# Kernel optimization log

Hardware: AMD Instinct MI355X
Metric: run time of the kernel (lower is better)

The kernel has to match this reference:

```python
import jax, jax.numpy as jnp
import numpy as np

N = 100000   # nodes
E = 400000   # edges
R = 237      # relations
D = 200      # feature dim (dims=[200,200,200])
B = 4096     # triple batch
L = 2        # num GAT layers
ALPHA = 0.01 # leaky-relu slope


def setup_inputs() -> dict:
    key = jax.random.key(0)
    ks = jax.random.split(key, 11)
    return dict(
        ent_embed=jax.random.normal(ks[0], (N, D), jnp.float32),
        rel_embed=jax.random.normal(ks[1], (R, D), jnp.float32),
        W_gat=jax.random.normal(ks[2], (L, D, D), jnp.float32) * 0.1,
        att_a=jax.random.normal(ks[3], (L, 2 * D), jnp.float32) * 0.1,
        W_hw=jax.random.normal(ks[4], (D, D), jnp.float32) * 0.1,
        b_hw=jax.random.normal(ks[5], (1, D), jnp.float32) * 0.1,
        edge_src=jax.random.randint(ks[6], (E,), 0, N),
        edge_dst=jax.random.randint(ks[7], (E,), 0, N),
        batch_h=jax.random.randint(ks[8], (B,), 0, N),
        batch_r=jax.random.randint(ks[9], (B,), 0, R),
        batch_t=jax.random.randint(ks[10], (B,), 0, N),
    )


def _gat_layer(x, W, a, src, dst):
    # x: [N,D], W: [D,D], a: [2D]
    Wh = x @ W                                  # [N,D]
    s_src = Wh @ a[:D]                          # [N] source score
    s_dst = Wh @ a[D:]                          # [N] dest score
    e = jax.nn.leaky_relu(s_src[src] + s_dst[dst], ALPHA)  # [E]
    # segment softmax over incoming edges of each destination node
    m = jax.ops.segment_max(e, dst, num_segments=N)
    m = jax.lax.stop_gradient(jnp.where(jnp.isfinite(m), m, 0.0))
    ex = jnp.exp(e - m[dst])
    denom = jax.ops.segment_sum(ex, dst, num_segments=N)
    att = ex / jnp.maximum(denom[dst], 1e-9)    # [E]
    out = jax.ops.segment_sum(att[:, None] * Wh[src], dst, num_segments=N)  # [N,D]
    return jax.nn.sigmoid(out)                  # act = torch.sigmoid, 1 head, concat=False


def reference(ent_embed, rel_embed, W_gat, att_a, W_hw, b_hw,
              edge_src, edge_dst, batch_h, batch_r, batch_t):
    x = ent_embed
    for i in range(L):
        gat_out = _gat_layer(x, W_gat[i], att_a[i], edge_src, edge_dst)
        # highway gate: sigma = sigmoid(x W + b); shared W,b across layers
        sigma = jax.nn.sigmoid(x @ W_hw + b_hw)
        x = sigma * gat_out + (1.0 - sigma) * x
    h = x[batch_h]
    r = rel_embed[batch_r]
    t = x[batch_t]
    return (h, r, t)
```

## Files before the change

### kernel.cpp

```cpp
#include <hip/hip_runtime.h>
#include <math.h>

#define NNODES 100000
#define NEDGES 400000
#define DIM    200
#define NB     4096
#define NL     2
#define ALPHA  0.01f
#define D4     (DIM/4)
#define NPAD   100096
#define KPAD   224
#define NKS    7
#define NCF    26
#define NBB    (2*NB)
#define NBLK   ((NNODES + 255) / 256)
#define SCAN_BPB 1024
#define NSB    ((NNODES + SCAN_BPB - 1) / SCAN_BPB)

typedef __attribute__((ext_vector_type(8))) short short8;
typedef __attribute__((ext_vector_type(4))) float f32x4;

__device__ __forceinline__ float sigm(float v) { return 1.0f / (1.0f + expf(-v)); }
__device__ __forceinline__ unsigned short f2bf(float f) {
    unsigned u = __float_as_uint(f);
    unsigned r = u + 0x7fff + ((u >> 16) & 1);
    return (unsigned short)(r >> 16);
}
__device__ __forceinline__ float bflo(unsigned u) { return __uint_as_float(u << 16); }
__device__ __forceinline__ float bfhi(unsigned u) { return __uint_as_float(u & 0xffff0000u); }

__global__ __launch_bounds__(256) void zero_k(int* __restrict__ deg, int* __restrict__ mask,
                                              int* __restrict__ lbbuf)
{
    int i = blockIdx.x * 256 + threadIdx.x;
    if (i < NNODES) { deg[i] = 0; mask[i] = 0; }
    if (i < 320) lbbuf[i] = 0;
}

__global__ void hist_k(const int* __restrict__ dst, int* __restrict__ deg)
{
    int e = blockIdx.x * blockDim.x + threadIdx.x;
    if (e < NEDGES) atomicAdd(&deg[dst[e]], 1);
}

template<int MODE>
__global__ __launch_bounds__(256) void scanlb_k(const int* __restrict__ in,
                                                int* __restrict__ state,
                                                int* __restrict__ ticket,
                                                int* __restrict__ o0,
                                                int* __restrict__ o1,
                                                int* __restrict__ o2)
{
    __shared__ int sbid;
    __shared__ int tmp[256];
    __shared__ int sexcl;
    int tid = threadIdx.x;
    if (tid == 0) sbid = atomicAdd(ticket, 1);
    __syncthreads();
    int bid = sbid;
    int base = bid * SCAN_BPB + tid * 4;

    int4 v4 = make_int4(0, 0, 0, 0);
    if (base + 3 < NNODES) v4 = *(const int4*)(in + base);
    else {
        if (base + 0 < NNODES) v4.x = in[base + 0];
        if (base + 1 < NNODES) v4.y = in[base + 1];
        if (base + 2 < NNODES) v4.z = in[base + 2];
    }
    int s1 = v4.x + v4.y, s2 = s1 + v4.z, s3 = s2 + v4.w;

    tmp[tid] = s3; __syncthreads();
#pragma unroll
    for (int off = 1; off < 256; off <<= 1) {
        int t = (tid >= off) ? tmp[tid - off] : 0;
        __syncthreads();
        tmp[tid] += t;
        __syncthreads();
    }
    int bexcl_t = tmp[tid] - s3;
    int btotal  = tmp[255];

    if (tid == 0) {
        int st = (bid == 0) ? ((2 << 30) | btotal) : ((1 << 30) | btotal);
        __hip_atomic_store(&state[bid], st, __ATOMIC_RELEASE, __HIP_MEMORY_SCOPE_AGENT);
        if (bid == 0) sexcl = 0;
    }
    if (bid > 0 && tid < 64) {
        int excl = 0;
        int pred = bid - 1;
        while (pred >= -64) {
            int idx = pred - tid;
            int s = (idx >= 0)
                ? __hip_atomic_load(&state[idx], __ATOMIC_ACQUIRE, __HIP_MEMORY_SCOPE_AGENT)
                : (2 << 30);
            int f = ((unsigned)s) >> 30;
            unsigned long long nv = __ballot(f == 0);
            unsigned long long iv = __ballot(f == 2);
            int firstnv = nv ? (__ffsll(nv) - 1) : 64;
            int firstiv = iv ? (__ffsll(iv) - 1) : 64;
            if (firstiv < firstnv) {
                int contrib = (tid <= firstiv) ? (s & 0x3FFFFFFF) : 0;
#pragma unroll
                for (int m = 32; m; m >>= 1) contrib += __shfl_xor(contrib, m, 64);
                excl += contrib;
                break;
            } else if (firstnv > 0) {
                int contrib = (tid < firstnv) ? (s & 0x3FFFFFFF) : 0;
#pragma unroll
                for (int m = 32; m; m >>= 1) contrib += __shfl_xor(contrib, m, 64);
                excl += contrib;
                pred -= firstnv;
            }
        }
        if (tid == 0) {
            __hip_atomic_store(&state[bid], (2 << 30) | (excl + btotal),
                               __ATOMIC_RELEASE, __HIP_MEMORY_SCOPE_AGENT);
            sexcl = excl;
        }
    }
    __syncthreads();
    int ex = sexcl + bexcl_t;

    if (MODE == 0) {
        int4 r = make_int4(ex, ex + v4.x, ex + s1, ex + s2);
        if (base + 3 < NNODES) {
            *(int4*)(o0 + base) = r;
            *(int4*)(o1 + base) = r;
        } else {
            if (base + 0 < NNODES) { o0[base + 0] = r.x; o1[base + 0] = r.x; }
            if (base + 1 < NNODES) { o0[base + 1] = r.y; o1[base + 1] = r.y; }
            if (base + 2 < NNODES) { o0[base + 2] = r.z; o1[base + 2] = r.z; }
        }
        if (bid == NSB - 1 && tid == 0) o0[NNODES] = NEDGES;
    } else {
        int vv[4] = { v4.x, v4.y, v4.z, v4.w };
        int ee[4] = { ex, ex + v4.x, ex + s1, ex + s2 };
#pragma unroll
        for (int j = 0; j < 4; ++j) {
            int idx = base + j;
            if (idx < NNODES) {
                if (vv[j]) { o0[ee[j]] = idx; o1[idx] = ee[j]; }
                if (idx == NNODES - 1) *o2 = ee[j] + vv[j];
            }
        }
    }
}

__global__ void scatter_k(const int* __restrict__ src, const int* __restrict__ dst,
                          int* __restrict__ cursor, int* __restrict__ csr_src)
{
    int e = blockIdx.x * blockDim.x + threadIdx.x;
    if (e >= NEDGES) return;
    int d = dst[e];
    int p = atomicAdd(&cursor[d], 1);
    csr_src[p] = src[e];
}

__global__ void mark_k(const int* __restrict__ bh, const int* __restrict__ bt,
                       const int* __restrict__ rs, const int* __restrict__ csr_src,
                       int* __restrict__ mask)
{
    int e = blockIdx.x * 256 + threadIdx.x;
    if (e >= NBB) return;
    int node = (e < NB) ? bh[e] : bt[e - NB];
    mask[node] = 1;
    int b = rs[node], en = rs[node + 1];
    for (int j = b; j < en; ++j) mask[csr_src[j]] = 1;
}

__global__ __launch_bounds__(256) void convscore_k(const float* __restrict__ xin,
                                                   const float* __restrict__ wvl,
                                                   unsigned short* __restrict__ ap,
                                                   float* __restrict__ s_src,
                                                   float* __restrict__ s_dst)
{
    int gt = blockIdx.x * 256 + threadIdx.x;
    int row = gt >> 5, hl = gt & 31;
    if (row >= NPAD) return;

    float ps = 0.f, pd = 0.f;
    if (hl < 28) {
        uint4 o = make_uint4(0u, 0u, 0u, 0u);
        if (row < NNODES && hl < 25) {
            size_t base = (size_t)row * D4 + hl * 2;
            float4 x0 = ((const float4*)xin)[base];
            float4 x1 = ((const float4*)xin)[base + 1];
            o.x = (unsigned)f2bf(x0.x) | ((unsigned)f2bf(x0.y) << 16);
            o.y = (unsigned)f2bf(x0.z) | ((unsigned)f2bf(x0.w) << 16);
            o.z = (unsigned)f2bf(x1.x) | ((unsigned)f2bf(x1.y) << 16);
            o.w = (unsigned)f2bf(x1.z) | ((unsigned)f2bf(x1.w) << 16);
            float4 s0 = ((const float4*)wvl)[hl * 2];
            float4 s1 = ((const float4*)wvl)[hl * 2 + 1];
            float4 d0 = ((const float4*)(wvl + DIM))[hl * 2];
            float4 d1 = ((const float4*)(wvl + DIM))[hl * 2 + 1];
            ps = x0.x*s0.x + x0.y*s0.y + x0.z*s0.z + x0.w*s0.w
               + x1.x*s1.x + x1.y*s1.y + x1.z*s1.z + x1.w*s1.w;
            pd = x0.x*d0.x + x0.y*d0.y + x0.z*d0.z + x0.w*d0.w
               + x1.x*d1.x + x1.y*d1.y + x1.z*d1.z + x1.w*d1.w;
        }
        ((uint4*)ap)[(size_t)row * 28 + hl] = o;
    }
#pragma unroll
    for (int m = 16; m; m >>= 1) {
        ps += __shfl_xor(ps, m, 32);
        pd += __shfl_xor(pd, m, 32);
    }
    if (hl == 0 && row < NNODES) { s_src[row] = ps; s_dst[row] = pd; }
}

__global__ __launch_bounds__(256) void prep_k(const float* __restrict__ Wg,
                                              const float* __restrict__ Whw,
                                              const float* __restrict__ aa,
                                              unsigned short* __restrict__ wp0,
                                              unsigned short* __restrict__ wp1,
                                              float* __restrict__ wv)
{
    int t0 = blockIdx.x * 256 + threadIdx.x;
    const int WP = NKS * NCF * 64;
    if (t0 < 2 * WP) {
        int pk = (t0 >= WP) ? 1 : 0;
        int t = t0 - pk * WP;
        const float* Wgl = Wg + (size_t)pk * DIM * DIM;
        unsigned short* wp = pk ? wp1 : wp0;
        int l = t & 63, cf = (t >> 6) % NCF, ks = t / (NCF * 64);
        int col = (cf % 13) * 16 + (l & 15);
        const float* W = (cf < 13) ? Wgl : Whw;
        unsigned rr[4];
#pragma unroll
        for (int j = 0; j < 4; ++j) {
            int ka = ks * 32 + (l >> 4) * 8 + 2 * j;
            float fa = (ka < DIM && col < DIM) ? W[ka * DIM + col] : 0.f;
            float fb = (ka + 1 < DIM && col < DIM) ? W[(ka + 1) * DIM + col] : 0.f;
            rr[j] = (unsigned)f2bf(fa) | ((unsigned)f2bf(fb) << 16);
        }
        ((uint4*)wp)[t] = make_uint4(rr[0], rr[1], rr[2], rr[3]);
    } else {
        int u = t0 - 2 * WP;
        if (u >= NL * 2 * DIM) return;
        int l = u / (2 * DIM), sd = (u / DIM) % 2, k = u % DIM;
        const float* W = Wg + (size_t)l * DIM * DIM + (size_t)k * DIM;
        const float* av = aa + (size_t)l * 2 * DIM + sd * DIM;
        float s = 0.f;
        for (int c = 0; c < DIM; ++c) s = fmaf(W[c], av[c], s);
        wv[u] = s;
    }
}

template<int CFBASE, int INDIRECT>
__global__ __launch_bounds__(448) void gemm_half_k(const unsigned short* __restrict__ Apack,
                                                   const unsigned short* __restrict__ Wpack,
                                                   const float* __restrict__ bhw,
                                                   unsigned short* __restrict__ outb,
                                                   const int* __restrict__ Lrow,
                                                   const int* __restrict__ nLp,
                                                   int nfix)
{
    int nrows = nLp ? *nLp : nfix;
    int rowbase = blockIdx.x * 32;
    if (rowbase >= nrows) return;

    int tid = threadIdx.x;
    int w = tid >> 6;
    int l = tid & 63;
    int cgrp = l >> 4, cidx = l & 15;
    int cf0 = CFBASE + 2 * w;
    int cf1 = CFBASE + 2 * w + 1;
    int cf1l = (cf1 < NCF) ? cf1 : (NCF - 1);

    const short8* Bp = (const short8*)Wpack + l;
    short8 b0[NKS], b1[NKS];
#pragma unroll
    for (int ks = 0; ks < NKS; ++ks) {
        b0[ks] = Bp[(ks * NCF + cf0) * 64];
        b1[ks] = Bp[(ks * NCF + cf1l) * 64];
    }

    int ar0 = rowbase + cidx, ar1 = rowbase + 16 + cidx;
    if (INDIRECT) {
        ar0 = Lrow[min(ar0, nrows - 1)];
        ar1 = Lrow[min(ar1, nrows - 1)];
    }
    const short8* Ap0 = (const short8*)(Apack + (size_t)ar0 * KPAD + cgrp * 8);
    const short8* Ap1 = (const short8*)(Apack + (size_t)ar1 * KPAD + cgrp * 8);

    f32x4 acc00 = (f32x4){0.f,0.f,0.f,0.f}, acc01 = acc00, acc10 = acc00, acc11 = acc00;

    short8 a0[2], a1[2];
    a0[0] = Ap0[0];
    a1[0] = Ap1[0];

#pragma unroll
    for (int ks = 0; ks < NKS; ++ks) {
        const int cur = ks & 1, nxt = cur ^ 1;
        if (ks + 1 < NKS) {
            a0[nxt] = Ap0[(ks + 1) * 4];
            a1[nxt] = Ap1[(ks + 1) * 4];
        }
        acc00 = __builtin_amdgcn_mfma_f32_16x16x32_bf16(a0[cur], b0[ks], acc00, 0, 0, 0);
        acc01 = __builtin_amdgcn_mfma_f32_16x16x32_bf16(a0[cur], b1[ks], acc01, 0, 0, 0);
        acc10 = __builtin_amdgcn_mfma_f32_16x16x32_bf16(a1[cur], b0[ks], acc10, 0, 0, 0);
        acc11 = __builtin_amdgcn_mfma_f32_16x16x32_bf16(a1[cur], b1[ks], acc11, 0, 0, 0);
    }

#pragma unroll
    for (int cc = 0; cc < 2; ++cc) {
        int cf = cc ? cf1 : cf0;
        if (cf >= CFBASE + 13) continue;
        int col = (cf - CFBASE) * 16 + cidx;
        if (col >= DIM) continue;
        f32x4 ar_0 = cc ? acc01 : acc00;
        f32x4 ar_1 = cc ? acc11 : acc10;
        if (CFBASE == 0) {
#pragma unroll
            for (int r = 0; r < 4; ++r) {
                int row = rowbase + cgrp * 4 + r;
                if (row < nrows) outb[(size_t)row * DIM + col] = f2bf(ar_0[r]);
                row += 16;
                if (row < nrows) outb[(size_t)row * DIM + col] = f2bf(ar_1[r]);
            }
        } else {
            float bb2 = bhw[col];
#pragma unroll
            for (int r = 0; r < 4; ++r) {
                int row = rowbase + cgrp * 4 + r;
                if (row < nrows) outb[(size_t)row * DIM + col] = f2bf(sigm(ar_0[r] + bb2));
                row += 16;
                if (row < nrows) outb[(size_t)row * DIM + col] = f2bf(sigm(ar_1[r] + bb2));
            }
        }
    }
}

__global__ __launch_bounds__(256) void agg3c_k(const int* __restrict__ csr_src,
                                               const int* __restrict__ rs,
                                               const float* __restrict__ s_src,
                                               const float* __restrict__ s_dst,
                                               const unsigned short* __restrict__ whb,
                                               const unsigned short* __restrict__ sgc,
                                               unsigned short* __restrict__ apack,
                                               const int* __restrict__ Lrow,
                                               const int* __restrict__ nLp,
                                               const float* __restrict__ wvn,
                                               float* __restrict__ o_ssrc,
                                               float* __restrict__ o_sdst)
{
    int gt = blockIdx.x * 256 + threadIdx.x;
    int lidx = gt >> 5;
    int hl = gt & 31;
    if (lidx >= *nLp) return;
    int node = Lrow[lidx];

    int beg = rs[node], end = rs[node + 1];
    float sd = s_dst[node];

    float m = -3.4e38f;
    for (int j = beg + hl; j < end; j += 32) {
        float v = s_src[csr_src[j]] + sd;
        v = v > 0.f ? v : ALPHA * v;
        m = fmaxf(m, v);
    }
#pragma unroll
    for (int s = 16; s; s >>= 1) m = fmaxf(m, __shfl_xor(m, s, 32));
    float sum = 0.f;
    for (int j = beg + hl; j < end; j += 32) {
        float v = s_src[csr_src[j]] + sd;
        v = v > 0.f ? v : ALPHA * v;
        sum += expf(v - m);
    }
#pragma unroll
    for (int s = 16; s; s >>= 1) sum += __shfl_xor(sum, s, 32);
    float inv_ = 1.f / fmaxf(sum, 1e-9f);

    float ps = 0.f, pd = 0.f;
    if (hl < 25) {
        float av[8] = {0.f, 0.f, 0.f, 0.f, 0.f, 0.f, 0.f, 0.f};
        int j = beg;
        for (; j + 1 < end; j += 2) {
            int n0 = csr_src[j], n1 = csr_src[j + 1];
            float v0 = s_src[n0] + sd, v1 = s_src[n1] + sd;
            v0 = v0 > 0.f ? v0 : ALPHA * v0;
            v1 = v1 > 0.f ? v1 : ALPHA * v1;
            float c0 = expf(v0 - m) * inv_, c1 = expf(v1 - m) * inv_;
            uint4 w0 = ((const uint4*)whb)[(size_t)n0 * 25 + hl];
            uint4 w1 = ((const uint4*)whb)[(size_t)n1 * 25 + hl];
            av[0] = fmaf(c0, bflo(w0.x), av[0]); av[0] = fmaf(c1, bflo(w1.x), av[0]);
            av[1] = fmaf(c0, bfhi(w0.x), av[1]); av[1] = fmaf(c1, bfhi(w1.x), av[1]);
            av[2] = fmaf(c0, bflo(w0.y), av[2]); av[2] = fmaf(c1, bflo(w1.y), av[2]);
            av[3] = fmaf(c0, bfhi(w0.y), av[3]); av[3] = fmaf(c1, bfhi(w1.y), av[3]);
            av[4] = fmaf(c0, bflo(w0.z), av[4]); av[4] = fmaf(c1, bflo(w1.z), av[4]);
            av[5] = fmaf(c0, bfhi(w0.z), av[5]); av[5] = fmaf(c1, bfhi(w1.z), av[5]);
            av[6] = fmaf(c0, bflo(w0.w), av[6]); av[6] = fmaf(c1, bflo(w1.w), av[6]);
            av[7] = fmaf(c0, bfhi(w0.w), av[7]); av[7] = fmaf(c1, bfhi(w1.w), av[7]);
        }
        if (j < end) {
            int n0 = csr_src[j];
            float v0 = s_src[n0] + sd;
            v0 = v0 > 0.f ? v0 : ALPHA * v0;
            float c0 = expf(v0 - m) * inv_;
            uint4 w0 = ((const uint4*)whb)[(size_t)n0 * 25 + hl];
            av[0] = fmaf(c0, bflo(w0.x), av[0]);
            av[1] = fmaf(c0, bfhi(w0.x), av[1]);
            av[2] = fmaf(c0, bflo(w0.y), av[2]);
            av[3] = fmaf(c0, bfhi(w0.y), av[3]);
            av[4] = fmaf(c0, bflo(w0.z), av[4]);
            av[5] = fmaf(c0, bfhi(w0.z), av[5]);
            av[6] = fmaf(c0, bflo(w0.w), av[6]);
            av[7] = fmaf(c0, bfhi(w0.w), av[7]);
        }

        uint4 sv = ((const uint4*)sgc)[(size_t)lidx * 25 + hl];
        uint4 xv = ((const uint4*)apack)[(size_t)node * 28 + hl];
        float4 o0, o1;
        float s0;
        s0 = bflo(sv.x); o0.x = s0 * sigm(av[0]) + (1.f - s0) * bflo(xv.x);
        s0 = bfhi(sv.x); o0.y = s0 * sigm(av[1]) + (1.f - s0) * bfhi(xv.x);
        s0 = bflo(sv.y); o0.z = s0 * sigm(av[2]) + (1.f - s0) * bflo(xv.y);
        s0 = bfhi(sv.y); o0.w = s0 * sigm(av[3]) + (1.f - s0) * bfhi(xv.y);
        s0 = bflo(sv.z); o1.x = s0 * sigm(av[4]) + (1.f - s0) * bflo(xv.z);
        s0 = bfhi(sv.z); o1.y = s0 * sigm(av[5]) + (1.f - s0) * bfhi(xv.z);
        s0 = bflo(sv.w); o1.z = s0 * sigm(av[6]) + (1.f - s0) * bflo(xv.w);
        s0 = bfhi(sv.w); o1.w = s0 * sigm(av[7]) + (1.f - s0) * bfhi(xv.w);

        unsigned r0 = (unsigned)f2bf(o0.x) | ((unsigned)f2bf(o0.y) << 16);
        unsigned r1 = (unsigned)f2bf(o0.z) | ((unsigned)f2bf(o0.w) << 16);
        unsigned r2 = (unsigned)f2bf(o1.x) | ((unsigned)f2bf(o1.y) << 16);
        unsigned r3 = (unsigned)f2bf(o1.z) | ((unsigned)f2bf(o1.w) << 16);
        ((uint4*)apack)[(size_t)node * 28 + hl] = make_uint4(r0, r1, r2, r3);

        float4 ws0 = ((const float4*)wvn)[hl * 2];
        float4 ws1 = ((const float4*)wvn)[hl * 2 + 1];
        float4 wd0 = ((const float4*)(wvn + DIM))[hl * 2];
        float4 wd1 = ((const float4*)(wvn + DIM))[hl * 2 + 1];
        ps = o0.x*ws0.x + o0.y*ws0.y + o0.z*ws0.z + o0.w*ws0.w
           + o1.x*ws1.x + o1.y*ws1.y + o1.z*ws1.z + o1.w*ws1.w;
        pd = o0.x*wd0.x + o0.y*wd0.y + o0.z*wd0.z + o0.w*wd0.w
           + o1.x*wd1.x + o1.y*wd1.y + o1.z*wd1.z + o1.w*wd1.w;
    }
#pragma unroll
    for (int s = 16; s; s >>= 1) {
        ps += __shfl_xor(ps, s, 32);
        pd += __shfl_xor(pd, s, 32);
    }
    if (hl == 0) { o_ssrc[node] = ps; o_sdst[node] = pd; }
}

__global__ __launch_bounds__(256) void gatherrel_k(const unsigned short* __restrict__ apack,
                                                   const int* __restrict__ bh,
                                                   const int* __restrict__ bt,
                                                   unsigned short* __restrict__ bx,
                                                   const float* __restrict__ rel,
                                                   const int* __restrict__ br,
                                                   float* __restrict__ out)
{
    int i = blockIdx.x * 256 + threadIdx.x;
    const int GX = NBB * 28;
    if (i < GX) {
        int e = i / 28, q = i - e * 28;
        int node = (e < NB) ? bh[e] : bt[e - NB];
        ((uint4*)bx)[i] = ((const uint4*)apack)[(size_t)node * 28 + q];
    } else {
        int u = i - GX;
        if (u >= NB * D4) return;
        int row = u / D4, c = u - row * D4;
        ((float4*)out)[(size_t)(NB + row) * D4 + c] =
            ((const float4*)rel)[(size_t)br[row] * D4 + c];
    }
}

__global__ __launch_bounds__(256) void agg4_k(const int* __restrict__ csr_src,
                                              const int* __restrict__ rs,
                                              const float* __restrict__ s_src,
                                              const float* __restrict__ s_dst,
                                              const unsigned short* __restrict__ whc,
                                              const int* __restrict__ inv,
                                              const unsigned short* __restrict__ sgbatch,
                                              const unsigned short* __restrict__ bxpack,
                                              const int* __restrict__ bh,
                                              const int* __restrict__ bt,
                                              float* __restrict__ out)
{
    int gt = blockIdx.x * 256 + threadIdx.x;
    int e = gt >> 5;
    int hl = gt & 31;
    if (e >= NBB) return;
    int node = (e < NB) ? bh[e] : bt[e - NB];
    int orow = (e < NB) ? e : (2 * NB + (e - NB));

    int beg = rs[node], end = rs[node + 1];
    float sd = s_dst[node];

    float m = -3.4e38f;
    for (int j = beg + hl; j < end; j += 32) {
        float v = s_src[csr_src[j]] + sd;
        v = v > 0.f ? v : ALPHA * v;
        m = fmaxf(m, v);
    }
#pragma unroll
    for (int s = 16; s; s >>= 1) m = fmaxf(m, __shfl_xor(m, s, 32));
    float sum = 0.f;
    for (int j = beg + hl; j < end; j += 32) {
        float v = s_src[csr_src[j]] + sd;
        v = v > 0.f ? v : ALPHA * v;
        sum += expf(v - m);
    }
#pragma unroll
    for (int s = 16; s; s >>= 1) sum += __shfl_xor(sum, s, 32);
    float inv_ = 1.f / fmaxf(sum, 1e-9f);

    if (hl < 25) {
        float av[8] = {0.f, 0.f, 0.f, 0.f, 0.f, 0.f, 0.f, 0.f};
        int j = beg;
        for (; j + 1 < end; j += 2) {
            int n0 = csr_src[j], n1 = csr_src[j + 1];
            float v0 = s_src[n0] + sd, v1 = s_src[n1] + sd;
            v0 = v0 > 0.f ? v0 : ALPHA * v0;
            v1 = v1 > 0.f ? v1 : ALPHA * v1;
            float c0 = expf(v0 - m) * inv_, c1 = expf(v1 - m) * inv_;
            uint4 w0 = ((const uint4*)whc)[(size_t)inv[n0] * 25 + hl];
            uint4 w1 = ((const uint4*)whc)[(size_t)inv[n1] * 25 + hl];
            av[0] = fmaf(c0, bflo(w0.x), av[0]); av[0] = fmaf(c1, bflo(w1.x), av[0]);
            av[1] = fmaf(c0, bfhi(w0.x), av[1]); av[1] = fmaf(c1, bfhi(w1.x), av[1]);
            av[2] = fmaf(c0, bflo(w0.y), av[2]); av[2] = fmaf(c1, bflo(w1.y), av[2]);
            av[3] = fmaf(c0, bfhi(w0.y), av[3]); av[3] = fmaf(c1, bfhi(w1.y), av[3]);
            av[4] = fmaf(c0, bflo(w0.z), av[4]); av[4] = fmaf(c1, bflo(w1.z), av[4]);
            av[5] = fmaf(c0, bfhi(w0.z), av[5]); av[5] = fmaf(c1, bfhi(w1.z), av[5]);
            av[6] = fmaf(c0, bflo(w0.w), av[6]); av[6] = fmaf(c1, bflo(w1.w), av[6]);
            av[7] = fmaf(c0, bfhi(w0.w), av[7]); av[7] = fmaf(c1, bfhi(w1.w), av[7]);
        }
        if (j < end) {
            int n0 = csr_src[j];
            float v0 = s_src[n0] + sd;
            v0 = v0 > 0.f ? v0 : ALPHA * v0;
            float c0 = expf(v0 - m) * inv_;
            uint4 w0 = ((const uint4*)whc)[(size_t)inv[n0] * 25 + hl];
            av[0] = fmaf(c0, bflo(w0.x), av[0]);
            av[1] = fmaf(c0, bfhi(w0.x), av[1]);
            av[2] = fmaf(c0, bflo(w0.y), av[2]);
            av[3] = fmaf(c0, bfhi(w0.y), av[3]);
            av[4] = fmaf(c0, bflo(w0.z), av[4]);
            av[5] = fmaf(c0, bfhi(w0.z), av[5]);
            av[6] = fmaf(c0, bflo(w0.w), av[6]);
            av[7] = fmaf(c0, bfhi(w0.w), av[7]);
        }

        uint4 sv = ((const uint4*)sgbatch)[(size_t)e * 25 + hl];
        uint4 xv = ((const uint4*)bxpack)[(size_t)e * 28 + hl];
        float4 o0, o1;
        float s0;
        s0 = bflo(sv.x); o0.x = s0 * sigm(av[0]) + (1.f - s0) * bflo(xv.x);
        s0 = bfhi(sv.x); o0.y = s0 * sigm(av[1]) + (1.f - s0) * bfhi(xv.x);
        s0 = bflo(sv.y); o0.z = s0 * sigm(av[2]) + (1.f - s0) * bflo(xv.y);
        s0 = bfhi(sv.y); o0.w = s0 * sigm(av[3]) + (1.f - s0) * bfhi(xv.y);
        s0 = bflo(sv.z); o1.x = s0 * sigm(av[4]) + (1.f - s0) * bflo(xv.z);
        s0 = bfhi(sv.z); o1.y = s0 * sigm(av[5]) + (1.f - s0) * bfhi(xv.z);
        s0 = bflo(sv.w); o1.z = s0 * sigm(av[6]) + (1.f - s0) * bflo(xv.w);
        s0 = bfhi(sv.w); o1.w = s0 * sigm(av[7]) + (1.f - s0) * bfhi(xv.w);

        size_t base = (size_t)orow * D4 + hl * 2;
        ((float4*)out)[base]     = o0;
        ((float4*)out)[base + 1] = o1;
    }
}

extern "C" void kernel_launch(void* const* d_in, const int* in_sizes, int n_in,
                              void* d_out, int out_size, void* d_ws, size_t ws_size,
                              hipStream_t stream)
{
    const float* ent = (const float*)d_in[0];
    const float* rel = (const float*)d_in[1];
    const float* Wg  = (const float*)d_in[2];
    const float* aa  = (const float*)d_in[3];
    const float* Whw = (const float*)d_in[4];
    const float* bhw = (const float*)d_in[5];
    const int* esrc  = (const int*)d_in[6];
    const int* edst  = (const int*)d_in[7];
    const int* bh    = (const int*)d_in[8];
    const int* br    = (const int*)d_in[9];
    const int* bt    = (const int*)d_in[10];
    float* out = (float*)d_out;

    char* p = (char*)d_ws;
    auto carve = [&](size_t bytes) { char* r = p; p += (bytes + 63) & ~(size_t)63; return r; };
    unsigned short* whb     = (unsigned short*)carve((size_t)NNODES * DIM * 2);
    unsigned short* whc     = (unsigned short*)carve((size_t)NNODES * DIM * 2);
    unsigned short* sgc     = (unsigned short*)carve((size_t)NNODES * DIM * 2);
    unsigned short* apack   = (unsigned short*)carve((size_t)NPAD * KPAD * 2);
    unsigned short* bxpack  = (unsigned short*)carve((size_t)NBB * KPAD * 2);
    unsigned short* sgbatch = (unsigned short*)carve((size_t)NBB * DIM * 2);
    unsigned short* wp0     = (unsigned short*)carve((size_t)NKS * NCF * 64 * 16);
    unsigned short* wp1     = (unsigned short*)carve((size_t)NKS * NCF * 64 * 16);
    float* wv    = (float*)carve(NL * 2 * DIM * 4);
    float* ss0   = (float*)carve(NNODES * 4);
    float* sd0   = (float*)carve(NNODES * 4);
    float* ss1   = (float*)carve(NNODES * 4);
    float* sd1   = (float*)carve(NNODES * 4);
    int* deg     = (int*)carve(NNODES * 4);
    int* rs      = (int*)carve((NNODES + 1) * 4);
    int* cursor  = (int*)carve(NNODES * 4);
    int* csr_src = (int*)carve(NEDGES * 4);
    int* mask    = (int*)carve(NNODES * 4);
    int* Lrow    = (int*)carve(NNODES * 4);
    int* inv     = (int*)carve(NNODES * 4);
    int* lbbuf   = (int*)carve(320 * 4);
    int* nLp     = (int*)carve(64);

    int* st0   = lbbuf;
    int* st1   = lbbuf + 128;
    int* tick0 = lbbuf + 256;
    int* tick1 = lbbuf + 257;

    zero_k<<<NBLK, 256, 0, stream>>>(deg, mask, lbbuf);
    hist_k<<<(NEDGES + 255) / 256, 256, 0, stream>>>(edst, deg);
    scanlb_k<0><<<NSB, 256, 0, stream>>>(deg, st0, tick0, rs, cursor, nullptr);
    scatter_k<<<(NEDGES + 255) / 256, 256, 0, stream>>>(esrc, edst, cursor, csr_src);
    mark_k<<<(NBB + 255) / 256, 256, 0, stream>>>(bh, bt, rs, csr_src, mask);
    scanlb_k<1><<<NSB, 256, 0, stream>>>(mask, st1, tick1, Lrow, inv, nLp);

    prep_k<<<(2 * NKS * NCF * 64 + NL * 2 * DIM + 255) / 256, 256, 0, stream>>>(
        Wg, Whw, aa, wp0, wp1, wv);

    convscore_k<<<(NPAD * 32) / 256, 256, 0, stream>>>(ent, wv, apack, ss0, sd0);

    const int GFULL = NPAD / 32;

    gemm_half_k<0, 0><<<GFULL, 448, 0, stream>>>(apack, wp0, bhw, whb, nullptr, nullptr, NNODES);
    gemm_half_k<13, 1><<<GFULL, 448, 0, stream>>>(apack, wp0, bhw, sgc, Lrow, nLp, 0);
    agg3c_k<<<(NNODES * 32) / 256, 256, 0, stream>>>(csr_src, rs, ss0, sd0, whb, sgc,
                                                     apack, Lrow, nLp, wv + 2 * DIM, ss1, sd1);

    gemm_half_k<0, 1><<<GFULL, 448, 0, stream>>>(apack, wp1, bhw, whc, Lrow, nLp, 0);
    gatherrel_k<<<(NBB * 28 + NB * D4 + 255) / 256, 256, 0, stream>>>(
        apack, bh, bt, bxpack, rel, br, out);
    gemm_half_k<13, 0><<<NBB / 32, 448, 0, stream>>>(bxpack, wp1, bhw, sgbatch, nullptr, nullptr, NBB);
    agg4_k<<<(NBB * 32) / 256, 256, 0, stream>>>(csr_src, rs, ss1, sd1, whc, inv,
                                                 sgbatch, bxpack, bh, bt, out);
}
```

Measured before the change: 224.5 us.

## Fuse small graph-prep kernels with GEMM slices to overlap CSR build and matmul

Merges zero/prep, convscore/histogram, and the CSR scan/scatter/mark steps into combined kernels, each carrying a quarter slice of the layer-0 GEMM blocks so the latency-bound graph-building work runs alongside MFMA work. The layer-0 highway gate GEMM is now computed for all nodes directly instead of only for marked rows. The batch gather into a separate packed buffer is replaced by indirect row indexing inside the GEMM and the final aggregation kernel. This cuts the number of launches and the extra copy, but it computes more highway-gate rows and mixes very different block types within a single launch.

Measured after the change: 227.5 us. Within noise of the previous version (+1.3%).

```diff
diff --git a/kernel.cpp b/kernel.cpp
--- a/kernel.cpp
+++ b/kernel.cpp
@@ -16,6 +16,16 @@
 #define NBLK   ((NNODES + 255) / 256)
 #define SCAN_BPB 1024
 #define NSB    ((NNODES + SCAN_BPB - 1) / SCAN_BPB)
+#define GFULL  (NPAD / 32)
+#define GEMM_TOT (2 * GFULL)
+#define SLICE  ((GEMM_TOT + 3) / 4)
+#define CSBLK  ((NPAD * 32) / 256)
+#define HBLK   ((NEDGES + 255) / 256)
+#define PREPBLK ((2 * NKS * NCF * 64 + NL * 2 * DIM + 255) / 256)
+#define SCATB  ((NEDGES + 447) / 448)
+#define MARKB  ((NBB + 447) / 448)
+#define SGB    (NBB / 32)
+#define RELB   ((NB * D4 + 447) / 448)
 
 typedef __attribute__((ext_vector_type(8))) short short8;
 typedef __attribute__((ext_vector_type(4))) float f32x4;
@@ -29,55 +39,40 @@
 __device__ __forceinline__ float bflo(unsigned u) { return __uint_as_float(u << 16); }
 __device__ __forceinline__ float bfhi(unsigned u) { return __uint_as_float(u & 0xffff0000u); }
 
-__global__ __launch_bounds__(256) void zero_k(int* __restrict__ deg, int* __restrict__ mask,
-                                              int* __restrict__ lbbuf)
-{
-    int i = blockIdx.x * 256 + threadIdx.x;
-    if (i < NNODES) { deg[i] = 0; mask[i] = 0; }
-    if (i < 320) lbbuf[i] = 0;
-}
-
-__global__ void hist_k(const int* __restrict__ dst, int* __restrict__ deg)
-{
-    int e = blockIdx.x * blockDim.x + threadIdx.x;
-    if (e < NEDGES) atomicAdd(&deg[dst[e]], 1);
-}
-
 template<int MODE>
-__global__ __launch_bounds__(256) void scanlb_k(const int* __restrict__ in,
-                                                int* __restrict__ state,
-                                                int* __restrict__ ticket,
-                                                int* __restrict__ o0,
-                                                int* __restrict__ o1,
-                                                int* __restrict__ o2)
+__device__ void scan_body(const int* __restrict__ in, int* __restrict__ state,
+                          int* __restrict__ ticket, int* __restrict__ o0,
+                          int* __restrict__ o1, int* __restrict__ o2, int tid)
 {
     __shared__ int sbid;
     __shared__ int tmp[256];
     __shared__ int sexcl;
-    int tid = threadIdx.x;
     if (tid == 0) sbid = atomicAdd(ticket, 1);
     __syncthreads();
     int bid = sbid;
     int base = bid * SCAN_BPB + tid * 4;
 
     int4 v4 = make_int4(0, 0, 0, 0);
-    if (base + 3 < NNODES) v4 = *(const int4*)(in + base);
-    else {
-        if (base + 0 < NNODES) v4.x = in[base + 0];
-        if (base + 1 < NNODES) v4.y = in[base + 1];
-        if (base + 2 < NNODES) v4.z = in[base + 2];
+    if (tid < 256) {
+        if (base + 3 < NNODES) v4 = *(const int4*)(in + base);
+        else {
+            if (base + 0 < NNODES) v4.x = in[base + 0];
+            if (base + 1 < NNODES) v4.y = in[base + 1];
+            if (base + 2 < NNODES) v4.z = in[base + 2];
+        }
     }
     int s1 = v4.x + v4.y, s2 = s1 + v4.z, s3 = s2 + v4.w;
 
-    tmp[tid] = s3; __syncthreads();
+    if (tid < 256) tmp[tid] = s3;
+    __syncthreads();
 #pragma unroll
     for (int off = 1; off < 256; off <<= 1) {
-        int t = (tid >= off) ? tmp[tid - off] : 0;
+        int t = (tid < 256 && tid >= off) ? tmp[tid - off] : 0;
         __syncthreads();
-        tmp[tid] += t;
+        if (tid < 256) tmp[tid] += t;
         __syncthreads();
     }
-    int bexcl_t = tmp[tid] - s3;
+    int bexcl_t = (tid < 256) ? (tmp[tid] - s3) : 0;
     int btotal  = tmp[255];
 
     if (tid == 0) {
@@ -121,62 +116,186 @@
     __syncthreads();
     int ex = sexcl + bexcl_t;
 
-    if (MODE == 0) {
-        int4 r = make_int4(ex, ex + v4.x, ex + s1, ex + s2);
-        if (base + 3 < NNODES) {
-            *(int4*)(o0 + base) = r;
-            *(int4*)(o1 + base) = r;
+    if (tid < 256) {
+        if (MODE == 0) {
+            int4 r = make_int4(ex, ex + v4.x, ex + s1, ex + s2);
+            if (base + 3 < NNODES) {
+                *(int4*)(o0 + base) = r;
+                *(int4*)(o1 + base) = r;
+            } else {
+                if (base + 0 < NNODES) { o0[base + 0] = r.x; o1[base + 0] = r.x; }
+                if (base + 1 < NNODES) { o0[base + 1] = r.y; o1[base + 1] = r.y; }
+                if (base + 2 < NNODES) { o0[base + 2] = r.z; o1[base + 2] = r.z; }
+            }
+            if (bid == NSB - 1 && tid == 0) o0[NNODES] = NEDGES;
         } else {
-            if (base + 0 < NNODES) { o0[base + 0] = r.x; o1[base + 0] = r.x; }
-            if (base + 1 < NNODES) { o0[base + 1] = r.y; o1[base + 1] = r.y; }
-            if (base + 2 < NNODES) { o0[base + 2] = r.z; o1[base + 2] = r.z; }
-        }
-        if (bid == NSB - 1 && tid == 0) o0[NNODES] = NEDGES;
+            int vv[4] = { v4.x, v4.y, v4.z, v4.w };
+            int ee[4] = { ex, ex + v4.x, ex + s1, ex + s2 };
+#pragma unroll
+            for (int j = 0; j < 4; ++j) {
+                int idx = base + j;
+                if (idx < NNODES) {
+                    if (vv[j]) { o0[ee[j]] = idx; o1[idx] = ee[j]; }
+                    if (idx == NNODES - 1) *o2 = ee[j] + vv[j];
+                }
+            }
+        }
+    }
+}
+
+template<int CFBASE, int IND>
+__device__ __forceinline__ void gemm_body(const unsigned short* __restrict__ Apack,
+                                          const unsigned short* __restrict__ Wpack,
+                                          const float* __restrict__ bhw,
+                                          unsigned short* __restrict__ outb,
+                                          const int* __restrict__ Lrow,
+                                          const int* __restrict__ bh,
+                                          const int* __restrict__ bt,
+                                          int nrows, int vb, int tid)
+{
+    int rowbase = vb * 32;
+    if (rowbase >= nrows) return;
+
+    int w = tid >> 6;
+    int l = tid & 63;
+    int cgrp = l >> 4, cidx = l & 15;
+    int cf0 = CFBASE + 2 * w;
+    int cf1 = CFBASE + 2 * w + 1;
+    int cf1l = (cf1 < NCF) ? cf1 : (NCF - 1);
+
+    const short8* Bp = (const short8*)Wpack + l;
+    short8 b0[NKS], b1[NKS];
+#pragma unroll
+    for (int ks = 0; ks < NKS; ++ks) {
+        b0[ks] = Bp[(ks * NCF + cf0) * 64];
+        b1[ks] = Bp[(ks * NCF + cf1l) * 64];
+    }
+
+    int e0 = rowbase + cidx, e1 = rowbase + 16 + cidx;
+    int ar0, ar1;
+    if (IND == 1) {
+        ar0 = Lrow[min(e0, nrows - 1)];
+        ar1 = Lrow[min(e1, nrows - 1)];
+    } else if (IND == 2) {
+        int c0 = min(e0, nrows - 1), c1 = min(e1, nrows - 1);
+        ar0 = (c0 < NB) ? bh[c0] : bt[c0 - NB];
+        ar1 = (c1 < NB) ? bh[c1] : bt[c1 - NB];
+    } else { ar0 = e0; ar1 = e1; }
+
+    const short8* Ap0 = (const short8*)(Apack + (size_t)ar0 * KPAD + cgrp * 8);
+    const short8* Ap1 = (const short8*)(Apack + (size_t)ar1 * KPAD + cgrp * 8);
+
+    f32x4 acc00 = (f32x4){0.f,0.f,0.f,0.f}, acc01 = acc00, acc10 = acc00, acc11 = acc00;
+
+    short8 a0[2], a1[2];
+    a0[0] = Ap0[0];
+    a1[0] = Ap1[0];
+
+#pragma unroll
+    for (int ks = 0; ks < NKS; ++ks) {
+        const int cur = ks & 1, nxt = cur ^ 1;
+        if (ks + 1 < NKS) {
+            a0[nxt] = Ap0[(ks + 1) * 4];
+            a1[nxt] = Ap1[(ks + 1) * 4];
+        }
+        acc00 = __builtin_amdgcn_mfma_f32_16x16x32_bf16(a0[cur], b0[ks], acc00, 0, 0, 0);
+        acc01 = __builtin_amdgcn_mfma_f32_16x16x32_bf16(a0[cur], b1[ks], acc01, 0, 0, 0);
+        acc10 = __builtin_amdgcn_mfma_f32_16x16x32_bf16(a1[cur], b0[ks], acc10, 0, 0, 0);
+        acc11 = __builtin_amdgcn_mfma_f32_16x16x32_bf16(a1[cur], b1[ks], acc11, 0, 0, 0);
+    }
+
+#pragma unroll
+    for (int cc = 0; cc < 2; ++cc) {
+        int cf = cc ? cf1 : cf0;
+        if (cf >= CFBASE + 13) continue;
+        int col = (cf - CFBASE) * 16 + cidx;
+        if (col >= DIM) continue;
+        f32x4 ar_0 = cc ? acc01 : acc00;
+        f32x4 ar_1 = cc ? acc11 : acc10;
+        if (CFBASE == 0) {
+#pragma unroll
+            for (int r = 0; r < 4; ++r) {
+                int row = rowbase + cgrp * 4 + r;
+                if (row < nrows) outb[(size_t)row * DIM + col] = f2bf(ar_0[r]);
+                row += 16;
+                if (row < nrows) outb[(size_t)row * DIM + col] = f2bf(ar_1[r]);
+            }
+        } else {
+            float bb2 = bhw[col];
+#pragma unroll
+            for (int r = 0; r < 4; ++r) {
+                int row = rowbase + cgrp * 4 + r;
+                if (row < nrows) outb[(size_t)row * DIM + col] = f2bf(sigm(ar_0[r] + bb2));
+                row += 16;
+                if (row < nrows) outb[(size_t)row * DIM + col] = f2bf(sigm(ar_1[r] + bb2));
+            }
+        }
+    }
+}
+
+__global__ __launch_bounds__(256) void zeroprep_k(int* __restrict__ deg, int* __restrict__ mask,
+                                                  int* __restrict__ lbbuf,
+                                                  const float* __restrict__ Wg,
+                                                  const float* __restrict__ Whw,
+                                                  const float* __restrict__ aa,
+                                                  unsigned short* __restrict__ wp0,
+                                                  unsigned short* __restrict__ wp1,
+                                                  float* __restrict__ wv)
+{
+    int bid = blockIdx.x, tid = threadIdx.x;
+    if (bid < NBLK) {
+        int i = bid * 256 + tid;
+        if (i < NNODES) { deg[i] = 0; mask[i] = 0; }
+        if (i < 320) lbbuf[i] = 0;
+        return;
+    }
+    int t0 = (bid - NBLK) * 256 + tid;
+    const int WP = NKS * NCF * 64;
+    if (t0 < 2 * WP) {
+        int pk = (t0 >= WP) ? 1 : 0;
+        int t = t0 - pk * WP;
+        const float* Wgl = Wg + (size_t)pk * DIM * DIM;
+        unsigned short* wp = pk ? wp1 : wp0;
+        int l = t & 63, cf = (t >> 6) % NCF, ks = t / (NCF * 64);
+        int col = (cf % 13) * 16 + (l & 15);
+        const float* W = (cf < 13) ? Wgl : Whw;
+        unsigned rr[4];
+#pragma unroll
+        for (int j = 0; j < 4; ++j) {
+            int ka = ks * 32 + (l >> 4) * 8 + 2 * j;
+            float fa = (ka < DIM && col < DIM) ? W[ka * DIM + col] : 0.f;
+            float fb = (ka + 1 < DIM && col < DIM) ? W[(ka + 1) * DIM + col] : 0.f;
+            rr[j] = (unsigned)f2bf(fa) | ((unsigned)f2bf(fb) << 16);
+        }
+        ((uint4*)wp)[t] = make_uint4(rr[0], rr[1], rr[2], rr[3]);
     } else {
-        int vv[4] = { v4.x, v4.y, v4.z, v4.w };
-        int ee[4] = { ex, ex + v4.x, ex + s1, ex + s2 };
-#pragma unroll
-        for (int j = 0; j < 4; ++j) {
-            int idx = base + j;
-            if (idx < NNODES) {
-                if (vv[j]) { o0[ee[j]] = idx; o1[idx] = ee[j]; }
-                if (idx == NNODES - 1) *o2 = ee[j] + vv[j];
-            }
-        }
-    }
-}
-
-__global__ void scatter_k(const int* __restrict__ src, const int* __restrict__ dst,
-                          int* __restrict__ cursor, int* __restrict__ csr_src)
-{
-    int e = blockIdx.x * blockDim.x + threadIdx.x;
-    if (e >= NEDGES) return;
-    int d = dst[e];
-    int p = atomicAdd(&cursor[d], 1);
-    csr_src[p] = src[e];
-}
-
-__global__ void mark_k(const int* __restrict__ bh, const int* __restrict__ bt,
-                       const int* __restrict__ rs, const int* __restrict__ csr_src,
-                       int* __restrict__ mask)
-{
-    int e = blockIdx.x * 256 + threadIdx.x;
-    if (e >= NBB) return;
-    int node = (e < NB) ? bh[e] : bt[e - NB];
-    mask[node] = 1;
-    int b = rs[node], en = rs[node + 1];
-    for (int j = b; j < en; ++j) mask[csr_src[j]] = 1;
-}
-
-__global__ __launch_bounds__(256) void convscore_k(const float* __restrict__ xin,
-                                                   const float* __restrict__ wvl,
-                                                   unsigned short* __restrict__ ap,
-                                                   float* __restrict__ s_src,
-                                                   float* __restrict__ s_dst)
-{
-    int gt = blockIdx.x * 256 + threadIdx.x;
+        int u = t0 - 2 * WP;
+        if (u >= NL * 2 * DIM) return;
+        int l = u / (2 * DIM), sd = (u / DIM) % 2, k = u % DIM;
+        const float* W = Wg + (size_t)l * DIM * DIM + (size_t)k * DIM;
+        const float* av = aa + (size_t)l * 2 * DIM + sd * DIM;
+        float s = 0.f;
+        for (int c = 0; c < DIM; ++c) s = fmaf(W[c], av[c], s);
+        wv[u] = s;
+    }
+}
+
+__global__ __launch_bounds__(256) void convhist_k(const float* __restrict__ xin,
+                                                  const float* __restrict__ wvl,
+                                                  unsigned short* __restrict__ ap,
+                                                  float* __restrict__ s_src,
+                                                  float* __restrict__ s_dst,
+                                                  const int* __restrict__ edst,
+                                                  int* __restrict__ deg)
+{
+    int bid = blockIdx.x, tid = threadIdx.x;
+    if (bid >= CSBLK) {
+        int e = (bid - CSBLK) * 256 + tid;
+        if (e < NEDGES) atomicAdd(&deg[edst[e]], 1);
+        return;
+    }
+    int gt = bid * 256 + tid;
     int row = gt >> 5, hl = gt & 31;
-    if (row >= NPAD) return;
 
     float ps = 0.f, pd = 0.f;
     if (hl < 28) {
@@ -208,127 +327,58 @@
     if (hl == 0 && row < NNODES) { s_src[row] = ps; s_dst[row] = pd; }
 }
 
-__global__ __launch_bounds__(256) void prep_k(const float* __restrict__ Wg,
-                                              const float* __restrict__ Whw,
-                                              const float* __restrict__ aa,
-                                              unsigned short* __restrict__ wp0,
-                                              unsigned short* __restrict__ wp1,
-                                              float* __restrict__ wv)
-{
-    int t0 = blockIdx.x * 256 + threadIdx.x;
-    const int WP = NKS * NCF * 64;
-    if (t0 < 2 * WP) {
-        int pk = (t0 >= WP) ? 1 : 0;
-        int t = t0 - pk * WP;
-        const float* Wgl = Wg + (size_t)pk * DIM * DIM;
-        unsigned short* wp = pk ? wp1 : wp0;
-        int l = t & 63, cf = (t >> 6) % NCF, ks = t / (NCF * 64);
-        int col = (cf % 13) * 16 + (l & 15);
-        const float* W = (cf < 13) ? Wgl : Whw;
-        unsigned rr[4];
-#pragma unroll
-        for (int j = 0; j < 4; ++j) {
-            int ka = ks * 32 + (l >> 4) * 8 + 2 * j;
-            float fa = (ka < DIM && col < DIM) ? W[ka * DIM + col] : 0.f;
-            float fb = (ka + 1 < DIM && col < DIM) ? W[(ka + 1) * DIM + col] : 0.f;
-            rr[j] = (unsigned)f2bf(fa) | ((unsigned)f2bf(fb) << 16);
-        }
-        ((uint4*)wp)[t] = make_uint4(rr[0], rr[1], rr[2], rr[3]);
-    } else {
-        int u = t0 - 2 * WP;
-        if (u >= NL * 2 * DIM) return;
-        int l = u / (2 * DIM), sd = (u / DIM) % 2, k = u % DIM;
-        const float* W = Wg + (size_t)l * DIM * DIM + (size_t)k * DIM;
-        const float* av = aa + (size_t)l * 2 * DIM + sd * DIM;
-        float s = 0.f;
-        for (int c = 0; c < DIM; ++c) s = fmaf(W[c], av[c], s);
-        wv[u] = s;
-    }
-}
-
-template<int CFBASE, int INDIRECT>
-__global__ __launch_bounds__(448) void gemm_half_k(const unsigned short* __restrict__ Apack,
-                                                   const unsigned short* __restrict__ Wpack,
-                                                   const float* __restrict__ bhw,
-                                                   unsigned short* __restrict__ outb,
-                                                   const int* __restrict__ Lrow,
-                                                   const int* __restrict__ nLp,
-                                                   int nfix)
-{
-    int nrows = nLp ? *nLp : nfix;
-    int rowbase = blockIdx.x * 32;
-    if (rowbase >= nrows) return;
-
-    int tid = threadIdx.x;
-    int w = tid >> 6;
-    int l = tid & 63;
-    int cgrp = l >> 4, cidx = l & 15;
-    int cf0 = CFBASE + 2 * w;
-    int cf1 = CFBASE + 2 * w + 1;
-    int cf1l = (cf1 < NCF) ? cf1 : (NCF - 1);
-
-    const short8* Bp = (const short8*)Wpack + l;
-    short8 b0[NKS], b1[NKS];
-#pragma unroll
-    for (int ks = 0; ks < NKS; ++ks) {
-        b0[ks] = Bp[(ks * NCF + cf0) * 64];
-        b1[ks] = Bp[(ks * NCF + cf1l) * 64];
-    }
-
-    int ar0 = rowbase + cidx, ar1 = rowbase + 16 + cidx;
-    if (INDIRECT) {
-        ar0 = Lrow[min(ar0, nrows - 1)];
-        ar1 = Lrow[min(ar1, nrows - 1)];
-    }
-    const short8* Ap0 = (const short8*)(Apack + (size_t)ar0 * KPAD + cgrp * 8);
-    const short8* Ap1 = (const short8*)(Apack + (size_t)ar1 * KPAD + cgrp * 8);
-
-    f32x4 acc00 = (f32x4){0.f,0.f,0.f,0.f}, acc01 = acc00, acc10 = acc00, acc11 = acc00;
-
-    short8 a0[2], a1[2];
-    a0[0] = Ap0[0];
-    a1[0] = Ap1[0];
-
-#pragma unroll
-    for (int ks = 0; ks < NKS; ++ks) {
-        const int cur = ks & 1, nxt = cur ^ 1;
-        if (ks + 1 < NKS) {
-            a0[nxt] = Ap0[(ks + 1) * 4];
-            a1[nxt] = Ap1[(ks + 1) * 4];
-        }
-        acc00 = __builtin_amdgcn_mfma_f32_16x16x32_bf16(a0[cur], b0[ks], acc00, 0, 0, 0);
-        acc01 = __builtin_amdgcn_mfma_f32_16x16x32_bf16(a0[cur], b1[ks], acc01, 0, 0, 0);
-        acc10 = __builtin_amdgcn_mfma_f32_16x16x32_bf16(a1[cur], b0[ks], acc10, 0, 0, 0);
-        acc11 = __builtin_amdgcn_mfma_f32_16x16x32_bf16(a1[cur], b1[ks], acc11, 0, 0, 0);
-    }
-
-#pragma unroll
-    for (int cc = 0; cc < 2; ++cc) {
-        int cf = cc ? cf1 : cf0;
-        if (cf >= CFBASE + 13) continue;
-        int col = (cf - CFBASE) * 16 + cidx;
-        if (col >= DIM) continue;
-        f32x4 ar_0 = cc ? acc01 : acc00;
-        f32x4 ar_1 = cc ? acc11 : acc10;
-        if (CFBASE == 0) {
-#pragma unroll
-            for (int r = 0; r < 4; ++r) {
-                int row = rowbase + cgrp * 4 + r;
-                if (row < nrows) outb[(size_t)row * DIM + col] = f2bf(ar_0[r]);
-                row += 16;
-                if (row < nrows) outb[(size_t)row * DIM + col] = f2bf(ar_1[r]);
+template<int PHASE>
+__global__ __launch_bounds__(448) void carrier_k(const int* __restrict__ sin,
+                                                 int* __restrict__ state,
+                                                 int* __restrict__ ticket,
+                                                 int* __restrict__ so0,
+                                                 int* __restrict__ so1,
+                                                 int* __restrict__ so2,
+                                                 const int* __restrict__ esrc,
+                                                 const int* __restrict__ edst,
+                                                 int* __restrict__ cursor,
+                                                 int* __restrict__ csr_src,
+                                                 const int* __restrict__ bh,
+                                                 const int* __restrict__ bt,
+                                                 const int* __restrict__ rs,
+                                                 int* __restrict__ mask,
+                                                 const unsigned short* __restrict__ Apack,
+                                                 const unsigned short* __restrict__ Wpack,
+                                                 const float* __restrict__ bhw,
+                                                 unsigned short* __restrict__ whb,
+                                                 unsigned short* __restrict__ sgc,
+                                                 int nsmall)
+{
+    int bid = blockIdx.x, tid = threadIdx.x;
+    if (bid < nsmall) {
+        if (PHASE == 0) {
+            scan_body<0>(sin, state, ticket, so0, so1, so2, tid);
+        } else if (PHASE == 3) {
+            scan_body<1>(sin, state, ticket, so0, so1, so2, tid);
+        } else if (PHASE == 1) {
+            int e = bid * 448 + tid;
+            if (e < NEDGES) {
+                int d = edst[e];
+                int p = atomicAdd(&cursor[d], 1);
+                csr_src[p] = esrc[e];
             }
         } else {
-            float bb2 = bhw[col];
-#pragma unroll
-            for (int r = 0; r < 4; ++r) {
-                int row = rowbase + cgrp * 4 + r;
-                if (row < nrows) outb[(size_t)row * DIM + col] = f2bf(sigm(ar_0[r] + bb2));
-                row += 16;
-                if (row < nrows) outb[(size_t)row * DIM + col] = f2bf(sigm(ar_1[r] + bb2));
+            int e = bid * 448 + tid;
+            if (e < NBB) {
+                int node = (e < NB) ? bh[e] : bt[e - NB];
+                mask[node] = 1;
+                int b = rs[node], en = rs[node + 1];
+                for (int j = b; j < en; ++j) mask[csr_src[j]] = 1;
             }
         }
-    }
+        return;
+    }
+    int vb = PHASE * SLICE + (bid - nsmall);
+    if (vb >= GEMM_TOT) return;
+    if (vb < GFULL)
+        gemm_body<0, 0>(Apack, Wpack, bhw, whb, nullptr, nullptr, nullptr, NNODES, vb, tid);
+    else
+        gemm_body<13, 0>(Apack, Wpack, bhw, sgc, nullptr, nullptr, nullptr, NNODES, vb - GFULL, tid);
 }
 
 __global__ __launch_bounds__(256) void agg3c_k(const int* __restrict__ csr_src,
@@ -408,7 +458,7 @@
             av[7] = fmaf(c0, bfhi(w0.w), av[7]);
         }
 
-        uint4 sv = ((const uint4*)sgc)[(size_t)lidx * 25 + hl];
+        uint4 sv = ((const uint4*)sgc)[(size_t)node * 25 + hl];
         uint4 xv = ((const uint4*)apack)[(size_t)node * 28 + hl];
         float4 o0, o1;
         float s0;
@@ -444,26 +494,31 @@
     if (hl == 0) { o_ssrc[node] = ps; o_sdst[node] = pd; }
 }
 
-__global__ __launch_bounds__(256) void gatherrel_k(const unsigned short* __restrict__ apack,
-                                                   const int* __restrict__ bh,
-                                                   const int* __restrict__ bt,
-                                                   unsigned short* __restrict__ bx,
-                                                   const float* __restrict__ rel,
-                                                   const int* __restrict__ br,
-                                                   float* __restrict__ out)
-{
-    int i = blockIdx.x * 256 + threadIdx.x;
-    const int GX = NBB * 28;
-    if (i < GX) {
-        int e = i / 28, q = i - e * 28;
-        int node = (e < NB) ? bh[e] : bt[e - NB];
-        ((uint4*)bx)[i] = ((const uint4*)apack)[(size_t)node * 28 + q];
+__global__ __launch_bounds__(448) void l1pack_k(const unsigned short* __restrict__ Apack,
+                                                const unsigned short* __restrict__ Wpack1,
+                                                const float* __restrict__ bhw,
+                                                unsigned short* __restrict__ whc,
+                                                unsigned short* __restrict__ sgbatch,
+                                                const int* __restrict__ Lrow,
+                                                const int* __restrict__ nLp,
+                                                const int* __restrict__ bh,
+                                                const int* __restrict__ bt,
+                                                const float* __restrict__ rel,
+                                                const int* __restrict__ br,
+                                                float* __restrict__ out)
+{
+    int bid = blockIdx.x, tid = threadIdx.x;
+    if (bid < GFULL) {
+        gemm_body<0, 1>(Apack, Wpack1, bhw, whc, Lrow, nullptr, nullptr, *nLp, bid, tid);
+    } else if (bid < GFULL + SGB) {
+        gemm_body<13, 2>(Apack, Wpack1, bhw, sgbatch, nullptr, bh, bt, NBB, bid - GFULL, tid);
     } else {
-        int u = i - GX;
-        if (u >= NB * D4) return;
-        int row = u / D4, c = u - row * D4;
-        ((float4*)out)[(size_t)(NB + row) * D4 + c] =
-            ((const float4*)rel)[(size_t)br[row] * D4 + c];
+        int u = (bid - GFULL - SGB) * 448 + tid;
+        if (u < NB * D4) {
+            int row = u / D4, c = u - row * D4;
+            ((float4*)out)[(size_t)(NB + row) * D4 + c] =
+                ((const float4*)rel)[(size_t)br[row] * D4 + c];
+        }
     }
 }
 
@@ -474,7 +529,7 @@
                                               const unsigned short* __restrict__ whc,
                                               const int* __restrict__ inv,
                                               const unsigned short* __restrict__ sgbatch,
-                                              const unsigned short* __restrict__ bxpack,
+                                              const unsigned short* __restrict__ apack,
                                               const int* __restrict__ bh,
                                               const int* __restrict__ bt,
                                               float* __restrict__ out)
@@ -544,7 +599,7 @@
         }
 
         uint4 sv = ((const uint4*)sgbatch)[(size_t)e * 25 + hl];
-        uint4 xv = ((const uint4*)bxpack)[(size_t)e * 28 + hl];
+        uint4 xv = ((const uint4*)apack)[(size_t)node * 28 + hl];
         float4 o0, o1;
         float s0;
         s0 = bflo(sv.x); o0.x = s0 * sigm(av[0]) + (1.f - s0) * bflo(xv.x);
@@ -585,7 +640,6 @@
     unsigned short* whc     = (unsigned short*)carve((size_t)NNODES * DIM * 2);
     unsigned short* sgc     = (unsigned short*)carve((size_t)NNODES * DIM * 2);
     unsigned short* apack   = (unsigned short*)carve((size_t)NPAD * KPAD * 2);
-    unsigned short* bxpack  = (unsigned short*)carve((size_t)NBB * KPAD * 2);
     unsigned short* sgbatch = (unsigned short*)carve((size_t)NBB * DIM * 2);
     unsigned short* wp0     = (unsigned short*)carve((size_t)NKS * NCF * 64 * 16);
     unsigned short* wp1     = (unsigned short*)carve((size_t)NKS * NCF * 64 * 16);
@@ -609,29 +663,26 @@
     int* tick0 = lbbuf + 256;
     int* tick1 = lbbuf + 257;
 
-    zero_k<<<NBLK, 256, 0, stream>>>(deg, mask, lbbuf);
-    hist_k<<<(NEDGES + 255) / 256, 256, 0, stream>>>(edst, deg);
-    scanlb_k<0><<<NSB, 256, 0, stream>>>(deg, st0, tick0, rs, cursor, nullptr);
-    scatter_k<<<(NEDGES + 255) / 256, 256, 0, stream>>>(esrc, edst, cursor, csr_src);
-    mark_k<<<(NBB + 255) / 256, 256, 0, stream>>>(bh, bt, rs, csr_src, mask);
-    scanlb_k<1><<<NSB, 256, 0, stream>>>(mask, st1, tick1, Lrow, inv, nLp);
-
-    prep_k<<<(2 * NKS * NCF * 64 + NL * 2 * DIM + 255) / 256, 256, 0, stream>>>(
-        Wg, Whw, aa, wp0, wp1, wv);
-
-    convscore_k<<<(NPAD * 32) / 256, 256, 0, stream>>>(ent, wv, apack, ss0, sd0);
-
-    const int GFULL = NPAD / 32;
-
-    gemm_half_k<0, 0><<<GFULL, 448, 0, stream>>>(apack, wp0, bhw, whb, nullptr, nullptr, NNODES);
-    gemm_half_k<13, 1><<<GFULL, 448, 0, stream>>>(apack, wp0, bhw, sgc, Lrow, nLp, 0);
+    zeroprep_k<<<NBLK + PREPBLK, 256, 0, stream>>>(deg, mask, lbbuf,
+                                                   Wg, Whw, aa, wp0, wp1, wv);
+
+    convhist_k<<<CSBLK + HBLK, 256, 0, stream>>>(ent, wv, apack, ss0, sd0, edst, deg);
+
+    carrier_k<0><<<NSB + SLICE, 448, 0, stream>>>(deg, st0, tick0, rs, cursor, nullptr,
+        esrc, edst, cursor, csr_src, bh, bt, rs, mask, apack, wp0, bhw, whb, sgc, NSB);
+    carrier_k<1><<<SCATB + SLICE, 448, 0, stream>>>(nullptr, nullptr, nullptr, nullptr, nullptr, nullptr,
+        esrc, edst, cursor, csr_src, bh, bt, rs, mask, apack, wp0, bhw, whb, sgc, SCATB);
+    carrier_k<2><<<MARKB + SLICE, 448, 0, stream>>>(nullptr, nullptr, nullptr, nullptr, nullptr, nullptr,
+        esrc, edst, cursor, csr_src, bh, bt, rs, mask, apack, wp0, bhw, whb, sgc, MARKB);
+    carrier_k<3><<<NSB + SLICE, 448, 0, stream>>>(mask, st1, tick1, Lrow, inv, nLp,
+        esrc, edst, cursor, csr_src, bh, bt, rs, mask, apack, wp0, bhw, whb, sgc, NSB);
+
     agg3c_k<<<(NNODES * 32) / 256, 256, 0, stream>>>(csr_src, rs, ss0, sd0, whb, sgc,
                                                      apack, Lrow, nLp, wv + 2 * DIM, ss1, sd1);
 
-    gemm_half_k<0, 1><<<GFULL, 448, 0, stream>>>(apack, wp1, bhw, whc, Lrow, nLp, 0);
-    gatherrel_k<<<(NBB * 28 + NB * D4 + 255) / 256, 256, 0, stream>>>(
-        apack, bh, bt, bxpack, rel, br, out);
-    gemm_half_k<13, 0><<<NBB / 32, 448, 0, stream>>>(bxpack, wp1, bhw, sgbatch, nullptr, nullptr, NBB);
+    l1pack_k<<<GFULL + SGB + RELB, 448, 0, stream>>>(apack, wp1, bhw, whc, sgbatch,
+                                                     Lrow, nLp, bh, bt, rel, br, out);
+
     agg4_k<<<(NBB * 32) / 256, 256, 0, stream>>>(csr_src, rs, ss1, sd1, whc, inv,
-                                                 sgbatch, bxpack, bh, bt, out);
-}
+                                                 sgbatch, apack, bh, bt, out);
+}
```
